# Performance work log

Hardware: AMD Instinct MI355X
Metric: run time of the kernel (lower is better)

## Reference

```python
import jax, jax.numpy as jnp
import numpy as np
from jax import lax

B, C_IN, C_OUT, KS, K, FD, L = 32, 128, 256, 9, 8, 64, 4096
PAD = KS // 2


def setup_inputs() -> dict:
    key = jax.random.key(0)
    ks = jax.random.split(key, 8)
    X = jax.random.normal(ks[0], (B, C_IN, L), dtype=jnp.float32)
    Z = jax.random.normal(ks[1], (B, FD), dtype=jnp.float32)
    # z_to_in: Linear(fluct_dim, in_planes), xavier-ish init, zero bias
    z_in_w = jax.random.normal(ks[2], (C_IN, FD), dtype=jnp.float32) * (1.0 / np.sqrt(FD))
    z_in_b = jnp.zeros((C_IN,), dtype=jnp.float32)
    # z_to_w MLP: in_planes -> in_planes//2 -> K
    w1 = jax.random.normal(ks[3], (C_IN // 2, C_IN), dtype=jnp.float32) * (1.0 / np.sqrt(C_IN))
    b1 = jax.random.normal(ks[4], (C_IN // 2,), dtype=jnp.float32) * 0.01
    w2 = jax.random.normal(ks[5], (K, C_IN // 2), dtype=jnp.float32) * (1.0 / np.sqrt(C_IN // 2))
    b2 = jax.random.normal(ks[6], (K,), dtype=jnp.float32) * 0.01
    weight_bank = jax.random.normal(ks[7], (K, C_OUT, C_IN, KS), dtype=jnp.float32) * (1.0 / np.sqrt(C_IN * KS))
    bias_bank = jnp.zeros((K, C_OUT), dtype=jnp.float32)
    return {"X": X, "Z": Z, "z_in_w": z_in_w, "z_in_b": z_in_b,
            "w1": w1, "b1": b1, "w2": w2, "b2": b2,
            "weight_bank": weight_bank, "bias_bank": bias_bank}


def _conv_one(x, w):
    # x: (C_in, L); w: (C_out, C_in, KS) -> (C_out, L)
    y = lax.conv_general_dilated(x[None], w, window_strides=(1,),
                                 padding=[(PAD, PAD)],
                                 dimension_numbers=("NCH", "OIH", "NCH"))
    return y[0]


def reference(X, Z, z_in_w, z_in_b, w1, b1, w2, b2, weight_bank, bias_bank):
    # routing: Z -> in_planes -> MLP -> softmax over K (dropout is inference no-op)
    proj = Z @ z_in_w.T + z_in_b                       # (B, C_in)
    h = jax.nn.relu(proj @ w1.T + b1)                  # (B, C_in//2)
    logits = h @ w2.T + b2                             # (B, K)
    omega = jax.nn.softmax(logits, axis=1)             # (B, K)
    # per-sample mixed kernels and biases
    W_tilde = jnp.einsum("bk,koci->boci", omega, weight_bank)  # (B, C_out, C_in, KS)
    b_tilde = omega @ bias_bank                         # (B, C_out)
    # batched per-sample conv (equiv. of the groups=B conv1d trick)
    Y = jax.vmap(_conv_one)(X, W_tilde)                 # (B, C_out, L)
    return Y + b_tilde[:, :, None]
```

## Files before the change

kernel.cpp:

```cpp
#include <hip/hip_runtime.h>
#include <math.h>

#define B_     32
#define C_INP  128
#define C_OUTP 256
#define KS_    9
#define KK_    8
#define FD_    64
#define LL_    4096
#define PAD_   4

#define LPAD   (LL_ + 2 * PAD_)

typedef unsigned short ushort_t;
typedef short bf16x8 __attribute__((ext_vector_type(8)));
typedef float f32x4 __attribute__((ext_vector_type(4)));

__device__ __forceinline__ ushort_t f2bf(float f) {
    unsigned u = __float_as_uint(f);
    unsigned r = (u + 0x7FFFu + ((u >> 16) & 1u)) >> 16;
    return (ushort_t)r;
}

__device__ __forceinline__ void gload16(const void* g, void* l) {
    __builtin_amdgcn_global_load_lds(
        (const __attribute__((address_space(1))) unsigned int*)g,
        (__attribute__((address_space(3))) unsigned int*)l, 16, 0, 0);
}

__global__ __launch_bounds__(256) void routing_kernel(
    const float* __restrict__ Z, const float* __restrict__ z_in_w,
    const float* __restrict__ z_in_b, const float* __restrict__ w1,
    const float* __restrict__ b1, const float* __restrict__ w2,
    const float* __restrict__ b2, const float* __restrict__ bias_bank,
    float* __restrict__ omega_out, float* __restrict__ btilde_out)
{
    const int b = blockIdx.x;
    const int tid = threadIdx.x;
    __shared__ float s_z[FD_];
    __shared__ float s_proj[C_INP];
    __shared__ float s_h[FD_];
    __shared__ float s_logits[KK_];
    __shared__ float s_omega[KK_];

    if (tid < FD_) s_z[tid] = Z[b * FD_ + tid];
    __syncthreads();

    if (tid < C_INP) {
        float acc = z_in_b[tid];
        const float* w = z_in_w + tid * FD_;
        #pragma unroll 8
        for (int f = 0; f < FD_; ++f) acc = fmaf(w[f], s_z[f], acc);
        s_proj[tid] = acc;
    }
    __syncthreads();

    if (tid < FD_) {
        float acc = b1[tid];
        const float* w = w1 + tid * C_INP;
        #pragma unroll 8
        for (int c = 0; c < C_INP; ++c) acc = fmaf(w[c], s_proj[c], acc);
        s_h[tid] = fmaxf(acc, 0.0f);
    }
    __syncthreads();

    if (tid < KK_) {
        float acc = b2[tid];
        const float* w = w2 + tid * FD_;
        #pragma unroll 8
        for (int j = 0; j < FD_; ++j) acc = fmaf(w[j], s_h[j], acc);
        s_logits[tid] = acc;
    }
    __syncthreads();

    if (tid == 0) {
        float m = s_logits[0];
        #pragma unroll
        for (int k = 1; k < KK_; ++k) m = fmaxf(m, s_logits[k]);
        float e[KK_];
        float s = 0.0f;
        #pragma unroll
        for (int k = 0; k < KK_; ++k) { e[k] = expf(s_logits[k] - m); s += e[k]; }
        const float inv = 1.0f / s;
        #pragma unroll
        for (int k = 0; k < KK_; ++k) s_omega[k] = e[k] * inv;
    }
    __syncthreads();

    if (tid < KK_) omega_out[b * KK_ + tid] = s_omega[tid];

    {
        float acc = 0.0f;
        #pragma unroll
        for (int k = 0; k < KK_; ++k) acc = fmaf(s_omega[k], bias_bank[k * C_OUTP + tid], acc);
        btilde_out[b * C_OUTP + tid] = acc;
    }
}

__global__ __launch_bounds__(256) void mix_kernel(
    const float* __restrict__ bank, const float* __restrict__ omega,
    ushort_t* __restrict__ wt)
{
    __shared__ float s_bank[KK_ * C_INP * KS_];
    __shared__ float s_om[B_ * KK_];

    const int o = blockIdx.x;
    const int tid = threadIdx.x;

    s_om[tid] = omega[tid];
    #pragma unroll
    for (int k = 0; k < KK_; ++k) {
        const float* src = bank + ((size_t)(k * C_OUTP + o)) * (C_INP * KS_);
        for (int i = tid; i < C_INP * KS_; i += 256)
            s_bank[k * (C_INP * KS_) + i] = src[i];
    }
    __syncthreads();

    for (int j = tid; j < KS_ * (C_INP / 2); j += 256) {
        const int t = j >> 6;
        const int c = (j & 63) * 2;
        float v0[KK_], v1[KK_];
        #pragma unroll
        for (int k = 0; k < KK_; ++k) {
            v0[k] = s_bank[k * (C_INP * KS_) + c * KS_ + t];
            v1[k] = s_bank[k * (C_INP * KS_) + (c + 1) * KS_ + t];
        }
        #pragma unroll
        for (int b = 0; b < B_; ++b) {
            float a0 = 0.0f, a1 = 0.0f;
            #pragma unroll
            for (int k = 0; k < KK_; ++k) {
                const float om = s_om[b * KK_ + k];
                a0 = fmaf(om, v0[k], a0);
                a1 = fmaf(om, v1[k], a1);
            }
            const unsigned packed = (unsigned)f2bf(a0) | ((unsigned)f2bf(a1) << 16);
            *(unsigned*)&wt[(((size_t)b * KS_ + t) * C_OUTP + o) * C_INP + c] = packed;
        }
    }
}

__global__ __launch_bounds__(256) void transpose_kernel(
    const float* __restrict__ X, ushort_t* __restrict__ XT)
{
    __shared__ ushort_t s_t[64 * 130];

    const int tid = threadIdx.x;
    const int l0 = blockIdx.x * 64;
    const int b = blockIdx.y;

    const int ll = tid & 63;
    const int cq = tid >> 6;
    const float* xb = X + ((size_t)b * C_INP) * LL_;

    #pragma unroll 4
    for (int r = 0; r < 32; ++r) {
        const int c = r * 4 + cq;
        s_t[ll * 130 + c] = f2bf(xb[(size_t)c * LL_ + l0 + ll]);
    }
    __syncthreads();

    ushort_t* xtb = XT + (size_t)b * LPAD * C_INP;
    for (int it = tid; it < 64 * 64; it += 256) {
        const int row = it >> 6;
        const int p = it & 63;
        const unsigned lo = s_t[row * 130 + p * 2];
        const unsigned hi = s_t[row * 130 + p * 2 + 1];
        *(unsigned*)(xtb + ((size_t)(4 + l0 + row)) * C_INP + p * 2) = lo | (hi << 16);
    }
    if (l0 == 0) {
        const int row = tid >> 6, p = tid & 63;
        *(unsigned*)(xtb + (size_t)row * C_INP + p * 2) = 0u;
    }
    if (l0 == LL_ - 64) {
        const int row = tid >> 6, p = tid & 63;
        *(unsigned*)(xtb + ((size_t)(LL_ + PAD_ + row)) * C_INP + p * 2) = 0u;
    }
}

__global__ __launch_bounds__(256, 2) void gemm_kernel(
    const ushort_t* __restrict__ XT, const ushort_t* __restrict__ WT,
    const float* __restrict__ btilde, float* __restrict__ Y)
{
    __shared__ __align__(16) ushort_t sX[136 * 128];
    __shared__ __align__(16) ushort_t sWr[4][128 * 32];

    const int tid = threadIdx.x;
    const int wid = tid >> 6;
    const int lane = tid & 63;

    const int wg = blockIdx.x;
    const int logical = (wg & 7) * 256 + (wg >> 3);
    const int b  = logical >> 6;
    const int rem = logical & 63;
    const int o0 = (rem >> 5) << 7;
    const int l0 = (rem & 31) << 7;

    const ushort_t* xtb = XT + ((size_t)b * LPAD + l0) * C_INP;
    const ushort_t* wtb = WT + ((size_t)b * KS_ * C_OUTP + o0) * C_INP;

    for (int g = tid; g < 2176; g += 256) {
        const int row = g >> 4;
        const int pcp = g & 15;
        gload16(xtb + row * C_INP + ((pcp ^ (row & 7)) * 8), sX + g * 8);
    }
    #pragma unroll
    for (int p = 0; p < 3; ++p) {
        ushort_t* wd = sWr[p];
        #pragma unroll
        for (int itr = 0; itr < 2; ++itr) {
            const int g = itr * 256 + tid;
            const int row = g >> 2;
            const int sp = g & 3;
            gload16(wtb + row * C_INP + p * 32 + ((sp ^ ((row >> 1) & 3)) * 8),
                    wd + g * 8);
        }
    }
    __syncthreads();

    const int ln15 = lane & 15;
    const int lh = lane >> 4;
    const int wm0 = (wid >> 1) * 64;
    const int wn0 = (wid & 1) * 64;

    f32x4 acc[4][4];
    #pragma unroll
    for (int i = 0; i < 4; ++i)
        #pragma unroll
        for (int j = 0; j < 4; ++j) acc[i][j] = (f32x4){0.f, 0.f, 0.f, 0.f};

    #pragma unroll 1
    for (int s = 0; s < 36; ++s) {
        const int t = s >> 2;
        const int q = s & 3;
        int s3 = s + 3; if (s3 >= 36) s3 -= 36;
        const ushort_t* wr = sWr[s & 3];
        ushort_t* wdst = sWr[s3 & 3];
        const ushort_t* wsrc = wtb + (size_t)(s3 >> 2) * (C_OUTP * C_INP) + (s3 & 3) * 32;

        bf16x8 a[4], bx[4];
        #pragma unroll
        for (int i = 0; i < 4; ++i) {
            const int arow = wm0 + i * 16 + ln15;
            a[i] = *(const bf16x8*)&sWr[s & 3][arow * 32 + ((lh ^ ((arow >> 1) & 3)) << 3)];
        }
        #pragma unroll
        for (int j = 0; j < 4; ++j) {
            const int brow = wn0 + t + j * 16 + ln15;
            bx[j] = *(const bf16x8*)&sX[brow * 128 + (((q * 4 + lh) ^ (brow & 7)) << 3)];
        }
        (void)wr;

        #pragma unroll
        for (int itr = 0; itr < 2; ++itr) {
            const int g = itr * 256 + tid;
            const int row = g >> 2;
            const int sp = g & 3;
            gload16(wsrc + row * C_INP + ((sp ^ ((row >> 1) & 3)) * 8), wdst + g * 8);
        }

        __builtin_amdgcn_s_setprio(1);
        #pragma unroll
        for (int i = 0; i < 4; ++i)
            #pragma unroll
            for (int j = 0; j < 4; ++j)
                acc[i][j] = __builtin_amdgcn_mfma_f32_16x16x32_bf16(
                    a[i], bx[j], acc[i][j], 0, 0, 0);
        __builtin_amdgcn_s_setprio(0);

        asm volatile("s_waitcnt vmcnt(4)" ::: "memory");
        __builtin_amdgcn_s_barrier();
        __builtin_amdgcn_sched_barrier(0);
    }
    asm volatile("s_waitcnt vmcnt(0)" ::: "memory");

    #pragma unroll
    for (int i = 0; i < 4; ++i) {
        const int obase = o0 + wm0 + i * 16 + lh * 4;
        const float4 bt = *(const float4*)&btilde[b * C_OUTP + obase];
        #pragma unroll
        for (int j = 0; j < 4; ++j) {
            const int lcol = l0 + wn0 + j * 16 + ln15;
            float* yp = Y + ((size_t)(b * C_OUTP + obase)) * LL_ + lcol;
            yp[0]           = acc[i][j][0] + bt.x;
            yp[LL_]         = acc[i][j][1] + bt.y;
            yp[2 * LL_]     = acc[i][j][2] + bt.z;
            yp[3 * LL_]     = acc[i][j][3] + bt.w;
        }
    }
}

#define O_TILE 8
#define T_PAD  12
__global__ __launch_bounds__(256) void conv_kernel(
    const float* __restrict__ X, const float* __restrict__ bank,
    const float* __restrict__ omega, const float* __restrict__ btilde,
    float* __restrict__ Y)
{
    __shared__ __align__(16) float s_w[C_INP * O_TILE * T_PAD];
    __shared__ float s_om[KK_];

    const int tid = threadIdx.x;
    const int o_base = blockIdx.x * O_TILE;
    const int b = blockIdx.y;

    if (tid < KK_) s_om[tid] = omega[b * KK_ + tid];
    __syncthreads();

    {
        const size_t kstride = (size_t)C_OUTP * C_INP * KS_;
        const float* bank_base = bank + (size_t)o_base * C_INP * KS_;
        for (int idx = tid; idx < O_TILE * C_INP * KS_; idx += 256) {
            const int o = idx / (C_INP * KS_);
            const int rem = idx - o * (C_INP * KS_);
            const int c = rem / KS_;
            const int t = rem - c * KS_;
            const float* p = bank_base + idx;
            float acc = 0.0f;
            #pragma unroll
            for (int k = 0; k < KK_; ++k) acc = fmaf(s_om[k], p[k * kstride], acc);
            s_w[(c * O_TILE + o) * T_PAD + t] = acc;
        }
    }
    __syncthreads();

    const int og = tid >> 7;
    const int lg = tid & 127;
    const float* xb = X + (size_t)b * C_INP * LL_;

    float bt[4];
    #pragma unroll
    for (int o = 0; o < 4; ++o) bt[o] = btilde[b * C_OUTP + o_base + og * 4 + o];

    for (int it = 0; it < 4; ++it) {
        const int l0 = it * 1024 + lg * 8;
        const int lx = l0 - PAD_;
        const bool fast = (lx >= 0) && (lx + 16 <= LL_);

        float acc[4][8];
        #pragma unroll
        for (int o = 0; o < 4; ++o)
            #pragma unroll
            for (int j = 0; j < 8; ++j) acc[o][j] = 0.0f;

        #pragma unroll 1
        for (int c = 0; c < C_INP; ++c) {
            const float* xrow = xb + (size_t)c * LL_;
            float x[16];
            if (fast) {
                const float4* p = reinterpret_cast<const float4*>(xrow + lx);
                const float4 a0 = p[0], a1 = p[1], a2 = p[2], a3 = p[3];
                x[0]=a0.x; x[1]=a0.y; x[2]=a0.z; x[3]=a0.w;
                x[4]=a1.x; x[5]=a1.y; x[6]=a1.z; x[7]=a1.w;
                x[8]=a2.x; x[9]=a2.y; x[10]=a2.z; x[11]=a2.w;
                x[12]=a3.x; x[13]=a3.y; x[14]=a3.z; x[15]=a3.w;
            } else {
                #pragma unroll
                for (int j = 0; j < 16; ++j) {
                    const int q = lx + j;
                    x[j] = (q >= 0 && q < LL_) ? xrow[q] : 0.0f;
                }
            }
            const float* wp = &s_w[(c * O_TILE + og * 4) * T_PAD];
            #pragma unroll
            for (int o = 0; o < 4; ++o) {
                #pragma unroll
                for (int t = 0; t < KS_; ++t) {
                    const float wv = wp[o * T_PAD + t];
                    #pragma unroll
                    for (int j = 0; j < 8; ++j)
                        acc[o][j] = fmaf(wv, x[j + t], acc[o][j]);
                }
            }
        }

        float* yb = Y + ((size_t)(b * C_OUTP + o_base + og * 4)) * LL_ + l0;
        #pragma unroll
        for (int o = 0; o < 4; ++o) {
            float4 r0, r1;
            r0.x = acc[o][0] + bt[o]; r0.y = acc[o][1] + bt[o];
            r0.z = acc[o][2] + bt[o]; r0.w = acc[o][3] + bt[o];
            r1.x = acc[o][4] + bt[o]; r1.y = acc[o][5] + bt[o];
            r1.z = acc[o][6] + bt[o]; r1.w = acc[o][7] + bt[o];
            float4* yp = reinterpret_cast<float4*>(yb + (size_t)o * LL_);
            yp[0] = r0; yp[1] = r1;
        }
    }
}

extern "C" void kernel_launch(void* const* d_in, const int* in_sizes, int n_in,
                              void* d_out, int out_size, void* d_ws, size_t ws_size,
                              hipStream_t stream)
{
    const float* X         = (const float*)d_in[0];
    const float* Z         = (const float*)d_in[1];
    const float* z_in_w    = (const float*)d_in[2];
    const float* z_in_b    = (const float*)d_in[3];
    const float* w1        = (const float*)d_in[4];
    const float* b1        = (const float*)d_in[5];
    const float* w2        = (const float*)d_in[6];
    const float* b2        = (const float*)d_in[7];
    const float* bank      = (const float*)d_in[8];
    const float* bias_bank = (const float*)d_in[9];
    float* out = (float*)d_out;

    char* ws = (char*)d_ws;
    float* omega  = (float*)ws;
    float* btilde = (float*)(ws + 1024);
    ushort_t* wt  = (ushort_t*)(ws + 1024 + 32768);
    ushort_t* XT  = (ushort_t*)(ws + 1024 + 32768 + (size_t)B_ * KS_ * C_OUTP * C_INP * 2);
    const size_t WS_NEEDED = 1024 + 32768
        + (size_t)B_ * KS_ * C_OUTP * C_INP * 2
        + (size_t)B_ * LPAD * C_INP * 2;

    routing_kernel<<<B_, 256, 0, stream>>>(Z, z_in_w, z_in_b, w1, b1, w2, b2,
                                           bias_bank, omega, btilde);

    if (ws_size >= WS_NEEDED) {
        mix_kernel<<<C_OUTP, 256, 0, stream>>>(bank, omega, wt);
        transpose_kernel<<<dim3(LL_ / 64, B_), 256, 0, stream>>>(X, XT);
        gemm_kernel<<<2048, 256, 0, stream>>>(XT, wt, btilde, out);
    } else {
        dim3 grid(C_OUTP / O_TILE, B_);
        conv_kernel<<<grid, 256, 0, stream>>>(X, bank, omega, btilde, out);
    }
}
```

Before: 127.5 us.

## Fuse routing, weight mixing and input transpose into one prep kernel

Replaces the routing, mix and transpose kernels with a single prep_kernel launch. Blocks 0-2047 transpose X to bf16, and blocks 2048-2303 each recompute the full routing MLP and softmax redundantly before mixing their output channel's weights. This removes two kernel launches and the serialization between routing and mixing, so the transpose can run alongside the mix. The cost is 256 redundant copies of the small routing MLP. The gemm kernel is moved and otherwise unchanged.

Measured after the change: 183.1 us. 43.6% more time.

```diff
diff --git a/kernel.cpp b/kernel.cpp
--- a/kernel.cpp
+++ b/kernel.cpp
@@ -26,6 +26,268 @@
     __builtin_amdgcn_global_load_lds(
         (const __attribute__((address_space(1))) unsigned int*)g,
         (__attribute__((address_space(3))) unsigned int*)l, 16, 0, 0);
+}
+
+__global__ __launch_bounds__(256) void prep_kernel(
+    const float* __restrict__ X, const float* __restrict__ Z,
+    const float* __restrict__ z_in_w, const float* __restrict__ z_in_b,
+    const float* __restrict__ w1, const float* __restrict__ b1,
+    const float* __restrict__ w2, const float* __restrict__ b2,
+    const float* __restrict__ bank, const float* __restrict__ bias_bank,
+    ushort_t* __restrict__ XT, ushort_t* __restrict__ wt,
+    float* __restrict__ btilde)
+{
+    __shared__ float s_buf[9216];
+    __shared__ float s_om[B_ * KK_];
+
+    const int bid = blockIdx.x;
+    const int tid = threadIdx.x;
+
+    if (bid < 2048) {
+        ushort_t* s_t = (ushort_t*)s_buf;
+        const int l0 = (bid & 63) * 64;
+        const int b = bid >> 6;
+
+        const int ll = tid & 63;
+        const int cq = tid >> 6;
+        const float* xb = X + ((size_t)b * C_INP) * LL_;
+
+        #pragma unroll 4
+        for (int r = 0; r < 32; ++r) {
+            const int c = r * 4 + cq;
+            s_t[ll * 130 + c] = f2bf(xb[(size_t)c * LL_ + l0 + ll]);
+        }
+        __syncthreads();
+
+        ushort_t* xtb = XT + (size_t)b * LPAD * C_INP;
+        for (int it = tid; it < 64 * 64; it += 256) {
+            const int row = it >> 6;
+            const int p = it & 63;
+            const unsigned lo = s_t[row * 130 + p * 2];
+            const unsigned hi = s_t[row * 130 + p * 2 + 1];
+            *(unsigned*)(xtb + ((size_t)(4 + l0 + row)) * C_INP + p * 2) = lo | (hi << 16);
+        }
+        if (l0 == 0) {
+            const int row = tid >> 6, p = tid & 63;
+            *(unsigned*)(xtb + (size_t)row * C_INP + p * 2) = 0u;
+        }
+        if (l0 == LL_ - 64) {
+            const int row = tid >> 6, p = tid & 63;
+            *(unsigned*)(xtb + ((size_t)(LL_ + PAD_ + row)) * C_INP + p * 2) = 0u;
+        }
+        return;
+    }
+
+    const int o = bid - 2048;
+
+    float* s_z    = s_buf;
+    float* s_proj = s_buf + 2048;
+    float* s_h    = s_buf + 6144;
+    float* s_lg   = s_buf + 8192;
+
+    for (int i = tid; i < B_ * FD_; i += 256) s_z[i] = Z[i];
+    __syncthreads();
+
+    for (int i = tid; i < B_ * C_INP; i += 256) {
+        const int b = i >> 7, c = i & 127;
+        float acc = z_in_b[c];
+        const float* w = z_in_w + c * FD_;
+        const float* zz = s_z + b * FD_;
+        #pragma unroll 8
+        for (int f = 0; f < FD_; ++f) acc = fmaf(w[f], zz[f], acc);
+        s_proj[i] = acc;
+    }
+    __syncthreads();
+
+    for (int i = tid; i < B_ * FD_; i += 256) {
+        const int b = i >> 6, j = i & 63;
+        float acc = b1[j];
+        const float* w = w1 + j * C_INP;
+        const float* pp = s_proj + b * C_INP;
+        #pragma unroll 8
+        for (int c = 0; c < C_INP; ++c) acc = fmaf(w[c], pp[c], acc);
+        s_h[i] = fmaxf(acc, 0.0f);
+    }
+    __syncthreads();
+
+    {
+        const int b = tid >> 3, k = tid & 7;
+        float acc = b2[k];
+        const float* w = w2 + k * FD_;
+        const float* hh = s_h + b * FD_;
+        #pragma unroll 8
+        for (int f = 0; f < FD_; ++f) acc = fmaf(w[f], hh[f], acc);
+        s_lg[tid] = acc;
+    }
+    __syncthreads();
+
+    if (tid < B_) {
+        const float* lg = s_lg + tid * KK_;
+        float m = lg[0];
+        #pragma unroll
+        for (int k = 1; k < KK_; ++k) m = fmaxf(m, lg[k]);
+        float e[KK_];
+        float ssum = 0.0f;
+        #pragma unroll
+        for (int k = 0; k < KK_; ++k) { e[k] = expf(lg[k] - m); ssum += e[k]; }
+        const float inv = 1.0f / ssum;
+        #pragma unroll
+        for (int k = 0; k < KK_; ++k) s_om[tid * KK_ + k] = e[k] * inv;
+    }
+    __syncthreads();
+
+    if (o == 0) {
+        for (int i = tid; i < B_ * C_OUTP; i += 256) {
+            const int b = i >> 8, oo = i & 255;
+            float acc = 0.0f;
+            #pragma unroll
+            for (int k = 0; k < KK_; ++k)
+                acc = fmaf(s_om[b * KK_ + k], bias_bank[k * C_OUTP + oo], acc);
+            btilde[i] = acc;
+        }
+    }
+
+    float* s_bank = s_buf;
+    #pragma unroll
+    for (int k = 0; k < KK_; ++k) {
+        const float* src = bank + ((size_t)(k * C_OUTP + o)) * (C_INP * KS_);
+        for (int i = tid; i < C_INP * KS_; i += 256)
+            s_bank[k * (C_INP * KS_) + i] = src[i];
+    }
+    __syncthreads();
+
+    for (int j = tid; j < KS_ * (C_INP / 2); j += 256) {
+        const int t = j >> 6;
+        const int c = (j & 63) * 2;
+        float v0[KK_], v1[KK_];
+        #pragma unroll
+        for (int k = 0; k < KK_; ++k) {
+            v0[k] = s_bank[k * (C_INP * KS_) + c * KS_ + t];
+            v1[k] = s_bank[k * (C_INP * KS_) + (c + 1) * KS_ + t];
+        }
+        #pragma unroll
+        for (int b = 0; b < B_; ++b) {
+            float a0 = 0.0f, a1 = 0.0f;
+            #pragma unroll
+            for (int k = 0; k < KK_; ++k) {
+                const float om = s_om[b * KK_ + k];
+                a0 = fmaf(om, v0[k], a0);
+                a1 = fmaf(om, v1[k], a1);
+            }
+            const unsigned packed = (unsigned)f2bf(a0) | ((unsigned)f2bf(a1) << 16);
+            *(unsigned*)&wt[(((size_t)b * KS_ + t) * C_OUTP + o) * C_INP + c] = packed;
+        }
+    }
+}
+
+__global__ __launch_bounds__(256, 2) void gemm_kernel(
+    const ushort_t* __restrict__ XT, const ushort_t* __restrict__ WT,
+    const float* __restrict__ btilde, float* __restrict__ Y)
+{
+    __shared__ __align__(16) ushort_t sX[136 * 128];
+    __shared__ __align__(16) ushort_t sWr[4][128 * 32];
+
+    const int tid = threadIdx.x;
+    const int wid = tid >> 6;
+    const int lane = tid & 63;
+
+    const int wg = blockIdx.x;
+    const int logical = (wg & 7) * 256 + (wg >> 3);
+    const int b  = logical >> 6;
+    const int rem = logical & 63;
+    const int o0 = (rem >> 5) << 7;
+    const int l0 = (rem & 31) << 7;
+
+    const ushort_t* xtb = XT + ((size_t)b * LPAD + l0) * C_INP;
+    const ushort_t* wtb = WT + ((size_t)b * KS_ * C_OUTP + o0) * C_INP;
+
+    for (int g = tid; g < 2176; g += 256) {
+        const int row = g >> 4;
+        const int pcp = g & 15;
+        gload16(xtb + row * C_INP + ((pcp ^ (row & 7)) * 8), sX + g * 8);
+    }
+    #pragma unroll
+    for (int p = 0; p < 3; ++p) {
+        ushort_t* wd = sWr[p];
+        #pragma unroll
+        for (int itr = 0; itr < 2; ++itr) {
+            const int g = itr * 256 + tid;
+            const int row = g >> 2;
+            const int sp = g & 3;
+            gload16(wtb + row * C_INP + p * 32 + ((sp ^ ((row >> 1) & 3)) * 8),
+                    wd + g * 8);
+        }
+    }
+    __syncthreads();
+
+    const int ln15 = lane & 15;
+    const int lh = lane >> 4;
+    const int wm0 = (wid >> 1) * 64;
+    const int wn0 = (wid & 1) * 64;
+
+    f32x4 acc[4][4];
+    #pragma unroll
+    for (int i = 0; i < 4; ++i)
+        #pragma unroll
+        for (int j = 0; j < 4; ++j) acc[i][j] = (f32x4){0.f, 0.f, 0.f, 0.f};
+
+    #pragma unroll 1
+    for (int s = 0; s < 36; ++s) {
+        const int t = s >> 2;
+        const int q = s & 3;
+        int s3 = s + 3; if (s3 >= 36) s3 -= 36;
+        ushort_t* wdst = sWr[s3 & 3];
+        const ushort_t* wsrc = wtb + (size_t)(s3 >> 2) * (C_OUTP * C_INP) + (s3 & 3) * 32;
+
+        bf16x8 a[4], bx[4];
+        #pragma unroll
+        for (int i = 0; i < 4; ++i) {
+            const int arow = wm0 + i * 16 + ln15;
+            a[i] = *(const bf16x8*)&sWr[s & 3][arow * 32 + ((lh ^ ((arow >> 1) & 3)) << 3)];
+        }
+        #pragma unroll
+        for (int j = 0; j < 4; ++j) {
+            const int brow = wn0 + t + j * 16 + ln15;
+            bx[j] = *(const bf16x8*)&sX[brow * 128 + (((q * 4 + lh) ^ (brow & 7)) << 3)];
+        }
+
+        #pragma unroll
+        for (int itr = 0; itr < 2; ++itr) {
+            const int g = itr * 256 + tid;
+            const int row = g >> 2;
+            const int sp = g & 3;
+            gload16(wsrc + row * C_INP + ((sp ^ ((row >> 1) & 3)) * 8), wdst + g * 8);
+        }
+
+        __builtin_amdgcn_s_setprio(1);
+        #pragma unroll
+        for (int i = 0; i < 4; ++i)
+            #pragma unroll
+            for (int j = 0; j < 4; ++j)
+                acc[i][j] = __builtin_amdgcn_mfma_f32_16x16x32_bf16(
+                    a[i], bx[j], acc[i][j], 0, 0, 0);
+        __builtin_amdgcn_s_setprio(0);
+
+        asm volatile("s_waitcnt vmcnt(4)" ::: "memory");
+        __builtin_amdgcn_s_barrier();
+        __builtin_amdgcn_sched_barrier(0);
+    }
+    asm volatile("s_waitcnt vmcnt(0)" ::: "memory");
+
+    #pragma unroll
+    for (int i = 0; i < 4; ++i) {
+        const int obase = o0 + wm0 + i * 16 + lh * 4;
+        const float4 bt = *(const float4*)&btilde[b * C_OUTP + obase];
+        #pragma unroll
+        for (int j = 0; j < 4; ++j) {
+            const int lcol = l0 + wn0 + j * 16 + ln15;
+            float* yp = Y + ((size_t)(b * C_OUTP + obase)) * LL_ + lcol;
+            yp[0]           = acc[i][j][0] + bt.x;
+            yp[LL_]         = acc[i][j][1] + bt.y;
+            yp[2 * LL_]     = acc[i][j][2] + bt.z;
+            yp[3 * LL_]     = acc[i][j][3] + bt.w;
+        }
+    }
 }
 
 __global__ __launch_bounds__(256) void routing_kernel(
@@ -94,199 +356,6 @@
         #pragma unroll
         for (int k = 0; k < KK_; ++k) acc = fmaf(s_omega[k], bias_bank[k * C_OUTP + tid], acc);
         btilde_out[b * C_OUTP + tid] = acc;
-    }
-}
-
-__global__ __launch_bounds__(256) void mix_kernel(
-    const float* __restrict__ bank, const float* __restrict__ omega,
-    ushort_t* __restrict__ wt)
-{
-    __shared__ float s_bank[KK_ * C_INP * KS_];
-    __shared__ float s_om[B_ * KK_];
-
-    const int o = blockIdx.x;
-    const int tid = threadIdx.x;
-
-    s_om[tid] = omega[tid];
-    #pragma unroll
-    for (int k = 0; k < KK_; ++k) {
-        const float* src = bank + ((size_t)(k * C_OUTP + o)) * (C_INP * KS_);
-        for (int i = tid; i < C_INP * KS_; i += 256)
-            s_bank[k * (C_INP * KS_) + i] = src[i];
-    }
-    __syncthreads();
-
-    for (int j = tid; j < KS_ * (C_INP / 2); j += 256) {
-        const int t = j >> 6;
-        const int c = (j & 63) * 2;
-        float v0[KK_], v1[KK_];
-        #pragma unroll
-        for (int k = 0; k < KK_; ++k) {
-            v0[k] = s_bank[k * (C_INP * KS_) + c * KS_ + t];
-            v1[k] = s_bank[k * (C_INP * KS_) + (c + 1) * KS_ + t];
-        }
-        #pragma unroll
-        for (int b = 0; b < B_; ++b) {
-            float a0 = 0.0f, a1 = 0.0f;
-            #pragma unroll
-            for (int k = 0; k < KK_; ++k) {
-                const float om = s_om[b * KK_ + k];
-                a0 = fmaf(om, v0[k], a0);
-                a1 = fmaf(om, v1[k], a1);
-            }
-            const unsigned packed = (unsigned)f2bf(a0) | ((unsigned)f2bf(a1) << 16);
-            *(unsigned*)&wt[(((size_t)b * KS_ + t) * C_OUTP + o) * C_INP + c] = packed;
-        }
-    }
-}
-
-__global__ __launch_bounds__(256) void transpose_kernel(
-    const float* __restrict__ X, ushort_t* __restrict__ XT)
-{
-    __shared__ ushort_t s_t[64 * 130];
-
-    const int tid = threadIdx.x;
-    const int l0 = blockIdx.x * 64;
-    const int b = blockIdx.y;
-
-    const int ll = tid & 63;
-    const int cq = tid >> 6;
-    const float* xb = X + ((size_t)b * C_INP) * LL_;
-
-    #pragma unroll 4
-    for (int r = 0; r < 32; ++r) {
-        const int c = r * 4 + cq;
-        s_t[ll * 130 + c] = f2bf(xb[(size_t)c * LL_ + l0 + ll]);
-    }
-    __syncthreads();
-
-    ushort_t* xtb = XT + (size_t)b * LPAD * C_INP;
-    for (int it = tid; it < 64 * 64; it += 256) {
-        const int row = it >> 6;
-        const int p = it & 63;
-        const unsigned lo = s_t[row * 130 + p * 2];
-        const unsigned hi = s_t[row * 130 + p * 2 + 1];
-        *(unsigned*)(xtb + ((size_t)(4 + l0 + row)) * C_INP + p * 2) = lo | (hi << 16);
-    }
-    if (l0 == 0) {
-        const int row = tid >> 6, p = tid & 63;
-        *(unsigned*)(xtb + (size_t)row * C_INP + p * 2) = 0u;
-    }
-    if (l0 == LL_ - 64) {
-        const int row = tid >> 6, p = tid & 63;
-        *(unsigned*)(xtb + ((size_t)(LL_ + PAD_ + row)) * C_INP + p * 2) = 0u;
-    }
-}
-
-__global__ __launch_bounds__(256, 2) void gemm_kernel(
-    const ushort_t* __restrict__ XT, const ushort_t* __restrict__ WT,
-    const float* __restrict__ btilde, float* __restrict__ Y)
-{
-    __shared__ __align__(16) ushort_t sX[136 * 128];
-    __shared__ __align__(16) ushort_t sWr[4][128 * 32];
-
-    const int tid = threadIdx.x;
-    const int wid = tid >> 6;
-    const int lane = tid & 63;
-
-    const int wg = blockIdx.x;
-    const int logical = (wg & 7) * 256 + (wg >> 3);
-    const int b  = logical >> 6;
-    const int rem = logical & 63;
-    const int o0 = (rem >> 5) << 7;
-    const int l0 = (rem & 31) << 7;
-
-    const ushort_t* xtb = XT + ((size_t)b * LPAD + l0) * C_INP;
-    const ushort_t* wtb = WT + ((size_t)b * KS_ * C_OUTP + o0) * C_INP;
-
-    for (int g = tid; g < 2176; g += 256) {
-        const int row = g >> 4;
-        const int pcp = g & 15;
-        gload16(xtb + row * C_INP + ((pcp ^ (row & 7)) * 8), sX + g * 8);
-    }
-    #pragma unroll
-    for (int p = 0; p < 3; ++p) {
-        ushort_t* wd = sWr[p];
-        #pragma unroll
-        for (int itr = 0; itr < 2; ++itr) {
-            const int g = itr * 256 + tid;
-            const int row = g >> 2;
-            const int sp = g & 3;
-            gload16(wtb + row * C_INP + p * 32 + ((sp ^ ((row >> 1) & 3)) * 8),
-                    wd + g * 8);
-        }
-    }
-    __syncthreads();
-
-    const int ln15 = lane & 15;
-    const int lh = lane >> 4;
-    const int wm0 = (wid >> 1) * 64;
-    const int wn0 = (wid & 1) * 64;
-
-    f32x4 acc[4][4];
-    #pragma unroll
-    for (int i = 0; i < 4; ++i)
-        #pragma unroll
-        for (int j = 0; j < 4; ++j) acc[i][j] = (f32x4){0.f, 0.f, 0.f, 0.f};
-
-    #pragma unroll 1
-    for (int s = 0; s < 36; ++s) {
-        const int t = s >> 2;
-        const int q = s & 3;
-        int s3 = s + 3; if (s3 >= 36) s3 -= 36;
-        const ushort_t* wr = sWr[s & 3];
-        ushort_t* wdst = sWr[s3 & 3];
-        const ushort_t* wsrc = wtb + (size_t)(s3 >> 2) * (C_OUTP * C_INP) + (s3 & 3) * 32;
-
-        bf16x8 a[4], bx[4];
-        #pragma unroll
-        for (int i = 0; i < 4; ++i) {
-            const int arow = wm0 + i * 16 + ln15;
-            a[i] = *(const bf16x8*)&sWr[s & 3][arow * 32 + ((lh ^ ((arow >> 1) & 3)) << 3)];
-        }
-        #pragma unroll
-        for (int j = 0; j < 4; ++j) {
-            const int brow = wn0 + t + j * 16 + ln15;
-            bx[j] = *(const bf16x8*)&sX[brow * 128 + (((q * 4 + lh) ^ (brow & 7)) << 3)];
-        }
-        (void)wr;
-
-        #pragma unroll
-        for (int itr = 0; itr < 2; ++itr) {
-            const int g = itr * 256 + tid;
-            const int row = g >> 2;
-            const int sp = g & 3;
-            gload16(wsrc + row * C_INP + ((sp ^ ((row >> 1) & 3)) * 8), wdst + g * 8);
-        }
-
-        __builtin_amdgcn_s_setprio(1);
-        #pragma unroll
-        for (int i = 0; i < 4; ++i)
-            #pragma unroll
-            for (int j = 0; j < 4; ++j)
-                acc[i][j] = __builtin_amdgcn_mfma_f32_16x16x32_bf16(
-                    a[i], bx[j], acc[i][j], 0, 0, 0);
-        __builtin_amdgcn_s_setprio(0);
-
-        asm volatile("s_waitcnt vmcnt(4)" ::: "memory");
-        __builtin_amdgcn_s_barrier();
-        __builtin_amdgcn_sched_barrier(0);
-    }
-    asm volatile("s_waitcnt vmcnt(0)" ::: "memory");
-
-    #pragma unroll
-    for (int i = 0; i < 4; ++i) {
-        const int obase = o0 + wm0 + i * 16 + lh * 4;
-        const float4 bt = *(const float4*)&btilde[b * C_OUTP + obase];
-        #pragma unroll
-        for (int j = 0; j < 4; ++j) {
-            const int lcol = l0 + wn0 + j * 16 + ln15;
-            float* yp = Y + ((size_t)(b * C_OUTP + obase)) * LL_ + lcol;
-            yp[0]           = acc[i][j][0] + bt.x;
-            yp[LL_]         = acc[i][j][1] + bt.y;
-            yp[2 * LL_]     = acc[i][j][2] + bt.z;
-            yp[3 * LL_]     = acc[i][j][3] + bt.w;
-        }
     }
 }
 
@@ -413,14 +482,14 @@
         + (size_t)B_ * KS_ * C_OUTP * C_INP * 2
         + (size_t)B_ * LPAD * C_INP * 2;
 
-    routing_kernel<<<B_, 256, 0, stream>>>(Z, z_in_w, z_in_b, w1, b1, w2, b2,
-                                           bias_bank, omega, btilde);
-
     if (ws_size >= WS_NEEDED) {
-        mix_kernel<<<C_OUTP, 256, 0, stream>>>(bank, omega, wt);
-        transpose_kernel<<<dim3(LL_ / 64, B_), 256, 0, stream>>>(X, XT);
+        prep_kernel<<<2304, 256, 0, stream>>>(X, Z, z_in_w, z_in_b, w1, b1,
+                                              w2, b2, bank, bias_bank,
+                                              XT, wt, btilde);
         gemm_kernel<<<2048, 256, 0, stream>>>(XT, wt, btilde, out);
     } else {
+        routing_kernel<<<B_, 256, 0, stream>>>(Z, z_in_w, z_in_b, w1, b1, w2, b2,
+                                               bias_bank, omega, btilde);
         dim3 grid(C_OUTP / O_TILE, B_);
         conv_kernel<<<grid, 256, 0, stream>>>(X, bank, omega, btilde, out);
     }
```
